# Kernel optimization log

Measured on AMD Instinct MI355X. Metric: run time of the kernel, lower is better.

## Reference

```python
import jax, jax.numpy as jnp
import numpy as np

SURROGATE_SCALE = 10.0  # SuperSpike-style surrogate slope

@jax.custom_vjp
def spike_fn(v):
    # Heaviside forward (standard SNN spike function)
    return (v > 0).astype(v.dtype)

def _spike_fwd(v):
    return spike_fn(v), v

def _spike_bwd(v, g):
    surrogate = 1.0 / (SURROGATE_SCALE * jnp.abs(v) + 1.0) ** 2
    return (g * surrogate,)

spike_fn.defvjp(_spike_fwd, _spike_bwd)

def setup_inputs() -> dict:
    key = jax.random.key(0)
    B, C, T = 128, 512, 1024
    x = jax.random.normal(key, (B, C, T), dtype=jnp.float32)
    beta = jnp.asarray(0.65, dtype=jnp.float32)   # scalar leak (non-trainable default)
    Vth = jnp.ones((C,), dtype=jnp.float32)        # threshold per channel
    return {"x": x, "beta": beta, "Vth": Vth}

def reference(x, beta, Vth):
    # x: (B, C, T)  -- time_position=2, negative_mempot=True, flatten_output=False
    B, C, T = x.shape
    xs = jnp.moveaxis(x, 2, 0)  # (T, B, C): scan over time

    def step(carry, inp):
        mem, spk = carry
        rst = spk * Vth                 # einsum('ab,b->ab', spk, Vth)
        mem = mem * beta + inp - rst    # negative_mempot branch
        spk = spike_fn(mem - Vth)
        return (mem, spk), spk

    init = (jnp.zeros((B, C), x.dtype), jnp.zeros((B, C), x.dtype))
    _, spk_rec = jax.lax.scan(step, init, xs)   # (T, B, C)
    return jnp.moveaxis(spk_rec, 0, 2)          # (B, C, T)
```

## Files before the change

### kernel.cpp

```cpp
#include <hip/hip_runtime.h>


#define LIF_B 128
#define LIF_C 512
#define LIF_T 1024

#define CHUNK 16
#define NCH   (LIF_T / CHUNK)

__global__ __launch_bounds__(256) void lif_fwd(
    const float* __restrict__ x,
    const float* __restrict__ beta_p,
    const float* __restrict__ vth_p,
    float* __restrict__ out)
{
    const int bc = blockIdx.x * 256 + threadIdx.x;
    const float beta = beta_p[0];
    const float vth  = vth_p[bc & (LIF_C - 1)];

    const float4* __restrict__ xv = (const float4*)(x   + (size_t)bc * LIF_T);
    float4*       __restrict__ ov = (float4*)      (out + (size_t)bc * LIF_T);

    float4 b0[4], b1[4];
#pragma unroll
    for (int j = 0; j < 4; ++j) b0[j] = xv[j];
#pragma unroll
    for (int j = 0; j < 4; ++j) b1[j] = xv[4 + j];

    float mem = 0.0f, spk = 0.0f;

    auto do_chunk = [&](float4 (&cb)[4], int ch) {
        float v[CHUNK];
#pragma unroll
        for (int j = 0; j < 4; ++j) {
            v[4 * j + 0] = cb[j].x;
            v[4 * j + 1] = cb[j].y;
            v[4 * j + 2] = cb[j].z;
            v[4 * j + 3] = cb[j].w;
        }
        const int pf = ch + 2;
        if (pf < NCH) {
#pragma unroll
            for (int j = 0; j < 4; ++j) cb[j] = xv[pf * 4 + j];
        }
        float o[CHUNK];
#pragma unroll
        for (int k = 0; k < CHUNK; ++k) {
            float rst = __fmul_rn(spk, vth);
            mem = __fsub_rn(__fadd_rn(__fmul_rn(mem, beta), v[k]), rst);
            spk = (__fsub_rn(mem, vth) > 0.0f) ? 1.0f : 0.0f;
            o[k] = spk;
        }
#pragma unroll
        for (int j = 0; j < 4; ++j) {
            float4 w;
            w.x = o[4 * j + 0];
            w.y = o[4 * j + 1];
            w.z = o[4 * j + 2];
            w.w = o[4 * j + 3];
            ov[ch * 4 + j] = w;
        }
    };

    for (int ch = 0; ch < NCH; ch += 2) {
        do_chunk(b0, ch);
        do_chunk(b1, ch + 1);
    }
}

extern "C" void kernel_launch(void* const* d_in, const int* in_sizes, int n_in,
                              void* d_out, int out_size, void* d_ws, size_t ws_size,
                              hipStream_t stream) {
    const float* x    = (const float*)d_in[0];
    const float* beta = (const float*)d_in[1];
    const float* vth  = (const float*)d_in[2];
    float* out = (float*)d_out;

    dim3 grid((LIF_B * LIF_C) / 256);
    lif_fwd<<<grid, 256, 0, stream>>>(x, beta, vth, out);
}
```

Measured before the change: 537.5 us.

## Stage time tiles through swizzled LDS for coalesced loads and stores

Each single-wave block now owns 64 rows and loads 64-step time tiles cooperatively, so each float4 load touches 16 consecutive addresses per row rather than one thread striding across a whole row. Tiles go into XOR-swizzled, double-buffered LDS; each lane runs the sequential LIF recurrence on its own row, writes the spikes back in place and the tile is stored coalesced. Register prefetch keeps the next two tiles in flight. The code has no barriers, relying on the block being a single wavefront. It also cuts occupancy per block and adds LDS traffic.

New measurement: 523.9 us. -2.5%, faster.

```diff
diff --git a/kernel.cpp b/kernel.cpp
--- a/kernel.cpp
+++ b/kernel.cpp
@@ -1,70 +1,108 @@
 #include <hip/hip_runtime.h>
 
 
-#define LIF_B 128
-#define LIF_C 512
-#define LIF_T 1024
+#define LIF_BC 65536
+#define LIF_T  1024
+#define TT     64
+#define NT     (LIF_T / TT)
+#define ROWS   64
 
-#define CHUNK 16
-#define NCH   (LIF_T / CHUNK)
-
-__global__ __launch_bounds__(256) void lif_fwd(
+__global__ __launch_bounds__(64) void lif_fwd(
     const float* __restrict__ x,
     const float* __restrict__ beta_p,
     const float* __restrict__ vth_p,
     float* __restrict__ out)
 {
-    const int bc = blockIdx.x * 256 + threadIdx.x;
+    __shared__ float lds[2][ROWS * TT];
+
+    const int lane = threadIdx.x;
+    const int r0   = blockIdx.x * ROWS;
+
     const float beta = beta_p[0];
-    const float vth  = vth_p[bc & (LIF_C - 1)];
+    const float vth  = vth_p[(r0 + lane) & 511];
 
-    const float4* __restrict__ xv = (const float4*)(x   + (size_t)bc * LIF_T);
-    float4*       __restrict__ ov = (float4*)      (out + (size_t)bc * LIF_T);
+    const int l_row4 = lane >> 4;
+    const int l_t    = lane & 15;
 
-    float4 b0[4], b1[4];
+    float4 pf[16];
+
+    auto issue_loads = [&](int tile) {
 #pragma unroll
-    for (int j = 0; j < 4; ++j) b0[j] = xv[j];
+        for (int j = 0; j < 16; ++j) {
+            const int row = 4 * j + l_row4;
+            pf[j] = *(const float4*)&x[(size_t)(r0 + row) * LIF_T
+                                       + (size_t)tile * TT + l_t * 4];
+        }
+    };
+
+    auto write_lds = [&](float* buf) {
 #pragma unroll
-    for (int j = 0; j < 4; ++j) b1[j] = xv[4 + j];
+        for (int j = 0; j < 16; ++j) {
+            const int row  = 4 * j + l_row4;
+            const int slot = l_t ^ (row & 15);
+            *(float4*)&buf[row * TT + slot * 4] = pf[j];
+        }
+    };
 
     float mem = 0.0f, spk = 0.0f;
 
-    auto do_chunk = [&](float4 (&cb)[4], int ch) {
-        float v[CHUNK];
+    auto compute = [&](float* buf) {
+        const int rbase = lane * TT;
+        const int sw    = lane & 15;
 #pragma unroll
-        for (int j = 0; j < 4; ++j) {
-            v[4 * j + 0] = cb[j].x;
-            v[4 * j + 1] = cb[j].y;
-            v[4 * j + 2] = cb[j].z;
-            v[4 * j + 3] = cb[j].w;
-        }
-        const int pf = ch + 2;
-        if (pf < NCH) {
-#pragma unroll
-            for (int j = 0; j < 4; ++j) cb[j] = xv[pf * 4 + j];
-        }
-        float o[CHUNK];
-#pragma unroll
-        for (int k = 0; k < CHUNK; ++k) {
-            float rst = __fmul_rn(spk, vth);
-            mem = __fsub_rn(__fadd_rn(__fmul_rn(mem, beta), v[k]), rst);
-            spk = (__fsub_rn(mem, vth) > 0.0f) ? 1.0f : 0.0f;
-            o[k] = spk;
-        }
-#pragma unroll
-        for (int j = 0; j < 4; ++j) {
-            float4 w;
-            w.x = o[4 * j + 0];
-            w.y = o[4 * j + 1];
-            w.z = o[4 * j + 2];
-            w.w = o[4 * j + 3];
-            ov[ch * 4 + j] = w;
+        for (int g = 0; g < 16; ++g) {
+            float4 v = *(float4*)&buf[rbase + (g ^ sw) * 4];
+            float o0, o1, o2, o3;
+            {
+                float rst = __fmul_rn(spk, vth);
+                mem = __fsub_rn(__fadd_rn(__fmul_rn(mem, beta), v.x), rst);
+                spk = (__fsub_rn(mem, vth) > 0.0f) ? 1.0f : 0.0f;
+                o0 = spk;
+            }
+            {
+                float rst = __fmul_rn(spk, vth);
+                mem = __fsub_rn(__fadd_rn(__fmul_rn(mem, beta), v.y), rst);
+                spk = (__fsub_rn(mem, vth) > 0.0f) ? 1.0f : 0.0f;
+                o1 = spk;
+            }
+            {
+                float rst = __fmul_rn(spk, vth);
+                mem = __fsub_rn(__fadd_rn(__fmul_rn(mem, beta), v.z), rst);
+                spk = (__fsub_rn(mem, vth) > 0.0f) ? 1.0f : 0.0f;
+                o2 = spk;
+            }
+            {
+                float rst = __fmul_rn(spk, vth);
+                mem = __fsub_rn(__fadd_rn(__fmul_rn(mem, beta), v.w), rst);
+                spk = (__fsub_rn(mem, vth) > 0.0f) ? 1.0f : 0.0f;
+                o3 = spk;
+            }
+            v.x = o0; v.y = o1; v.z = o2; v.w = o3;
+            *(float4*)&buf[rbase + (g ^ sw) * 4] = v;
         }
     };
 
-    for (int ch = 0; ch < NCH; ch += 2) {
-        do_chunk(b0, ch);
-        do_chunk(b1, ch + 1);
+    auto store_tile = [&](const float* buf, int tile) {
+#pragma unroll
+        for (int j = 0; j < 16; ++j) {
+            const int row  = 4 * j + l_row4;
+            const int slot = l_t ^ (row & 15);
+            float4 s = *(const float4*)&buf[row * TT + slot * 4];
+            *(float4*)&out[(size_t)(r0 + row) * LIF_T
+                           + (size_t)tile * TT + l_t * 4] = s;
+        }
+    };
+
+    issue_loads(0);
+    write_lds(lds[0]);
+    issue_loads(1);
+
+    for (int k = 0; k < NT; ++k) {
+        float* cur = lds[k & 1];
+        compute(cur);
+        if (k + 1 < NT) write_lds(lds[(k + 1) & 1]);
+        if (k + 2 < NT) issue_loads(k + 2);
+        store_tile(cur, k);
     }
 }
 
@@ -76,6 +114,6 @@
     const float* vth  = (const float*)d_in[2];
     float* out = (float*)d_out;
 
-    dim3 grid((LIF_B * LIF_C) / 256);
-    lif_fwd<<<grid, 256, 0, stream>>>(x, beta, vth, out);
+    dim3 grid(LIF_BC / ROWS);
+    lif_fwd<<<grid, 64, 0, stream>>>(x, beta, vth, out);
 }
```

## Warp-specialize LIF kernel with LDS ring buffer, async loads, and flag sync

Applied to the files above, without the earlier changes.

Splits each 512-thread block into compute, loader and storer wavefronts. The loaders bring 32-step time tiles of 256 rows into a 4-deep swizzled LDS ring using global_load_lds, and the storers write the spikes back with coalesced nontemporal stores. The aim is to replace strided per-thread row loads, where each thread reads its own 4KB row, with coalesced tile transfers that overlap the serial recurrence. In exchange it adds spin-wait synchronization on LDS atomics, 128KB of shared memory per block, and fewer resident blocks.

Result: faster. 482.8 us (-10.2%).

```diff
diff --git a/kernel.cpp b/kernel.cpp
--- a/kernel.cpp
+++ b/kernel.cpp
@@ -1,70 +1,114 @@
 #include <hip/hip_runtime.h>
 
 
-#define LIF_B 128
-#define LIF_C 512
-#define LIF_T 1024
+#define LIF_T   1024
+#define TT      32
+#define NTILES  (LIF_T / TT)
+#define RPB     256
+#define NBUF    4
+#define BUF_FLOATS (RPB * TT)
 
-#define CHUNK 16
-#define NCH   (LIF_T / CHUNK)
+using fvec4 = __attribute__((ext_vector_type(4))) float;
 
-__global__ __launch_bounds__(256) void lif_fwd(
+__global__ __launch_bounds__(512) void lif_fwd(
     const float* __restrict__ x,
     const float* __restrict__ beta_p,
     const float* __restrict__ vth_p,
     float* __restrict__ out)
 {
-    const int bc = blockIdx.x * 256 + threadIdx.x;
-    const float beta = beta_p[0];
-    const float vth  = vth_p[bc & (LIF_C - 1)];
+    __shared__ float buf[NBUF][BUF_FLOATS];
+    __shared__ int ready_flag[NBUF];
+    __shared__ int done_cnt[NBUF];
+    __shared__ int free_cnt[NBUF];
 
-    const float4* __restrict__ xv = (const float4*)(x   + (size_t)bc * LIF_T);
-    float4*       __restrict__ ov = (float4*)      (out + (size_t)bc * LIF_T);
+    const int tid  = threadIdx.x;
+    const int lane = tid & 63;
+    const int wid  = tid >> 6;
+    const int r0   = blockIdx.x * RPB;
 
-    float4 b0[4], b1[4];
+    if (tid < NBUF) { ready_flag[tid] = 0; done_cnt[tid] = 0; free_cnt[tid] = 0; }
+    __syncthreads();
+
+    if (wid < 4) {
+        const int   r    = (wid << 6) | lane;
+        const float beta = beta_p[0];
+        const float vth  = vth_p[(r0 + r) & 511];
+        const int   sw   = r & 7;
+        float mem = 0.0f, spk = 0.0f;
+
+        for (int k = 0; k < NTILES; ++k) {
+            const int b = k & (NBUF - 1);
+            while (__hip_atomic_load(&ready_flag[b], __ATOMIC_ACQUIRE,
+                                     __HIP_MEMORY_SCOPE_WORKGROUP) != k + 1)
+                __builtin_amdgcn_s_sleep(1);
+
+            float* rowp = &buf[b][r * TT];
 #pragma unroll
-    for (int j = 0; j < 4; ++j) b0[j] = xv[j];
+            for (int g = 0; g < 8; ++g) {
+                fvec4 v = *(fvec4*)&rowp[(g ^ sw) << 2];
 #pragma unroll
-    for (int j = 0; j < 4; ++j) b1[j] = xv[4 + j];
+                for (int e = 0; e < 4; ++e) {
+                    float rst = __fmul_rn(spk, vth);
+                    mem = __fsub_rn(__fadd_rn(__fmul_rn(mem, beta), v[e]), rst);
+                    spk = (__fsub_rn(mem, vth) > 0.0f) ? 1.0f : 0.0f;
+                    v[e] = spk;
+                }
+                *(fvec4*)&rowp[(g ^ sw) << 2] = v;
+            }
+            if (lane == 0)
+                __hip_atomic_fetch_add(&done_cnt[b], 1, __ATOMIC_RELEASE,
+                                       __HIP_MEMORY_SCOPE_WORKGROUP);
+        }
+    } else if (wid < 6) {
+        const int par = wid - 4;
+        const int jr  = lane >> 3;
+        const int g   = (lane & 7) ^ jr;
 
-    float mem = 0.0f, spk = 0.0f;
+        for (int k = par; k < NTILES; k += 2) {
+            const int b = k & (NBUF - 1);
+            while (__hip_atomic_load(&free_cnt[b], __ATOMIC_ACQUIRE,
+                                     __HIP_MEMORY_SCOPE_WORKGROUP) != (k >> 2))
+                __builtin_amdgcn_s_sleep(1);
 
-    auto do_chunk = [&](float4 (&cb)[4], int ch) {
-        float v[CHUNK];
 #pragma unroll
-        for (int j = 0; j < 4; ++j) {
-            v[4 * j + 0] = cb[j].x;
-            v[4 * j + 1] = cb[j].y;
-            v[4 * j + 2] = cb[j].z;
-            v[4 * j + 3] = cb[j].w;
+            for (int j = 0; j < 32; ++j) {
+                const int r = (j << 3) | jr;
+                const float* gsrc =
+                    &x[(size_t)(r0 + r) * LIF_T + k * TT + (g << 2)];
+                __builtin_amdgcn_global_load_lds(
+                    (const __attribute__((address_space(1))) unsigned int*)gsrc,
+                    (__attribute__((address_space(3))) unsigned int*)&buf[b][j << 8],
+                    16, 0, 2);
+            }
+            __builtin_amdgcn_s_waitcnt(0);
+            if (lane == 0)
+                __hip_atomic_store(&ready_flag[b], k + 1, __ATOMIC_RELEASE,
+                                   __HIP_MEMORY_SCOPE_WORKGROUP);
         }
-        const int pf = ch + 2;
-        if (pf < NCH) {
+    } else {
+        const int par = wid - 6;
+        const int jr  = lane >> 3;
+        const int gp  = (lane & 7) ^ jr;
+
+        for (int k = par; k < NTILES; k += 2) {
+            const int b    = k & (NBUF - 1);
+            const int want = ((k >> 2) + 1) * 4;
+            while (__hip_atomic_load(&done_cnt[b], __ATOMIC_ACQUIRE,
+                                     __HIP_MEMORY_SCOPE_WORKGROUP) != want)
+                __builtin_amdgcn_s_sleep(1);
+
 #pragma unroll
-            for (int j = 0; j < 4; ++j) cb[j] = xv[pf * 4 + j];
+            for (int j = 0; j < 32; ++j) {
+                const int r = (j << 3) | jr;
+                fvec4 s = *(fvec4*)&buf[b][r * TT + (gp << 2)];
+                __builtin_nontemporal_store(
+                    s, (fvec4*)&out[(size_t)(r0 + r) * LIF_T + k * TT
+                                    + ((lane & 7) << 2)]);
+            }
+            if (lane == 0)
+                __hip_atomic_fetch_add(&free_cnt[b], 1, __ATOMIC_RELEASE,
+                                       __HIP_MEMORY_SCOPE_WORKGROUP);
         }
-        float o[CHUNK];
-#pragma unroll
-        for (int k = 0; k < CHUNK; ++k) {
-            float rst = __fmul_rn(spk, vth);
-            mem = __fsub_rn(__fadd_rn(__fmul_rn(mem, beta), v[k]), rst);
-            spk = (__fsub_rn(mem, vth) > 0.0f) ? 1.0f : 0.0f;
-            o[k] = spk;
-        }
-#pragma unroll
-        for (int j = 0; j < 4; ++j) {
-            float4 w;
-            w.x = o[4 * j + 0];
-            w.y = o[4 * j + 1];
-            w.z = o[4 * j + 2];
-            w.w = o[4 * j + 3];
-            ov[ch * 4 + j] = w;
-        }
-    };
-
-    for (int ch = 0; ch < NCH; ch += 2) {
-        do_chunk(b0, ch);
-        do_chunk(b1, ch + 1);
     }
 }
 
@@ -76,6 +120,6 @@
     const float* vth  = (const float*)d_in[2];
     float* out = (float*)d_out;
 
-    dim3 grid((LIF_B * LIF_C) / 256);
-    lif_fwd<<<grid, 256, 0, stream>>>(x, beta, vth, out);
+    dim3 grid(65536 / RPB);
+    lif_fwd<<<grid, 512, 0, stream>>>(x, beta, vth, out);
 }
```
